# Kernel tuning notes

Hardware: AMD Instinct MI355X
Metric: run time of the kernel (lower is better)

Reference implementation:

```python
import jax, jax.numpy as jnp
import numpy as np

BOARD_H, BOARD_W = 10, 9
NUM_NODES = BOARD_H * BOARD_W  # 90
NUM_HEADS = 4


def _build_base_adjacency():
    adj = np.zeros((NUM_NODES, NUM_NODES), dtype=np.float32)
    for y in range(BOARD_H):
        for x in range(BOARD_W):
            idx = y * BOARD_W + x
            for dy, dx in [(0, 1), (0, -1), (1, 0), (-1, 0)]:
                ny, nx = y + dy, x + dx
                if 0 <= ny < BOARD_H and 0 <= nx < BOARD_W:
                    adj[idx, ny * BOARD_W + nx] = 1.0
            for nx in range(BOARD_W):
                if nx != x and abs(nx - x) <= 4:
                    nidx = y * BOARD_W + nx
                    adj[idx, nidx] = max(adj[idx, nidx], 1.0 / abs(nx - x))
            for ny in range(BOARD_H):
                if ny != y and abs(ny - y) <= 5:
                    nidx = ny * BOARD_W + x
                    adj[idx, nidx] = max(adj[idx, nidx], 1.0 / abs(ny - y))
            adj[idx, idx] = 1.0
    deg = np.clip(adj.sum(-1, keepdims=True), 1.0, None)
    return adj / deg  # (90, 90)


def _pos_encoding():
    px = (np.arange(BOARD_W, dtype=np.float32) / BOARD_W)
    py = (np.arange(BOARD_H, dtype=np.float32) / BOARD_H)
    gx = np.broadcast_to(px[None, :], (BOARD_H, BOARD_W)).reshape(-1)
    gy = np.broadcast_to(py[:, None], (BOARD_H, BOARD_W)).reshape(-1)
    return np.stack([gx, gy], axis=-1)  # (90, 2)


def _gat_layer(x, adj, W, a_src, a_dst, gamma, beta):
    B, N, _ = x.shape
    h = (x @ W).reshape(B, N, NUM_HEADS, -1)          # (B,N,H,D)
    s_src = jnp.einsum('bnhd,hd->bhn', h, a_src)       # (B,H,N)
    s_dst = jnp.einsum('bnhd,hd->bhn', h, a_dst)
    attn = s_src[..., :, None] + s_dst[..., None, :]   # (B,H,N,N)
    attn = jax.nn.leaky_relu(attn, 0.2)
    attn = jnp.where((adj == 0)[None, None], -jnp.inf, attn)
    attn = jax.nn.softmax(attn, axis=-1)
    attn = jnp.nan_to_num(attn, nan=0.0)
    out = jnp.einsum('bhij,bjhd->bihd', attn, h).reshape(B * N, -1)
    # BatchNorm1d in training mode: biased batch stats over (B*N)
    mean = out.mean(0)
    var = out.var(0)
    out = (out - mean) * jax.lax.rsqrt(var + 1e-5) * gamma + beta
    return jax.nn.relu(out.reshape(B, N, -1))


def setup_inputs() -> dict:
    key = jax.random.key(0)
    ks = jax.random.split(key, 16)
    B, F_in, Hd, Dout = 2048, 16, 64, 128
    hdim = Hd // NUM_HEADS
    p = lambda k, s: (jax.random.normal(k, s, dtype=jnp.float32) * 0.1)
    return {
        'board_planes': jax.random.uniform(ks[0], (B, 14, BOARD_H, BOARD_W), dtype=jnp.float32),
        'in_W': p(ks[1], (F_in, Hd)), 'in_b': p(ks[2], (Hd,)),
        'W0': p(ks[3], (Hd, Hd)), 'asrc0': p(ks[4], (NUM_HEADS, hdim)), 'adst0': p(ks[5], (NUM_HEADS, hdim)),
        'g0': jnp.ones((Hd,), jnp.float32), 'b0': jnp.zeros((Hd,), jnp.float32),
        'W1': p(ks[6], (Hd, Hd)), 'asrc1': p(ks[7], (NUM_HEADS, hdim)), 'adst1': p(ks[8], (NUM_HEADS, hdim)),
        'g1': jnp.ones((Hd,), jnp.float32), 'b1': jnp.zeros((Hd,), jnp.float32),
        'out_W': p(ks[9], (Hd, Dout)), 'out_b': p(ks[10], (Dout,)),
    }


def reference(board_planes, in_W, in_b, W0, asrc0, adst0, g0, b0,
              W1, asrc1, adst1, g1, b1, out_W, out_b):
    B = board_planes.shape[0]
    adj = jnp.asarray(_build_base_adjacency())            # (90,90), same for all batches
    nodes = board_planes.reshape(B, 14, NUM_NODES).transpose(0, 2, 1)  # (B,90,14)
    pos = jnp.broadcast_to(jnp.asarray(_pos_encoding())[None], (B, NUM_NODES, 2))
    x = jnp.concatenate([nodes, pos], axis=-1)            # (B,90,16)
    x = x @ in_W + in_b
    x = _gat_layer(x, adj, W0, asrc0, adst0, g0, b0)
    x = _gat_layer(x, adj, W1, asrc1, adst1, g1, b1)
    return x.mean(axis=1) @ out_W + out_b                 # (B,128)
```

## Files before the change

kernel.cpp:

```cpp
#include <hip/hip_runtime.h>
#include <cstdint>


#define BB   2048
#define NN   90
#define NP   96
#define CC   64
#define NH   4
#define HD   16
#define TPB  512
#define DOUT 128
#define SXP  72
#define SWP  72
#define PPITCH 20
#define NSLOT 19

typedef _Float16 f16;
typedef _Float16 f16x4 __attribute__((ext_vector_type(4)));
typedef _Float16 f16x8 __attribute__((ext_vector_type(8)));
typedef float f32x4 __attribute__((ext_vector_type(4)));
union U16x4 { f16x4 v; f16 e[4]; };
union U16x8 { f16x8 v; f16 e[8]; };


template <int LAYER>
__global__ __launch_bounds__(TPB, 6) void k_gat(
    const float* __restrict__ bp,
    const float* __restrict__ inW,
    const float* __restrict__ inb,
    const f16*   __restrict__ prevPre,
    const float* __restrict__ stPrev,
    const float* __restrict__ Wl,
    const float* __restrict__ asrc,
    const float* __restrict__ adst,
    f16*   __restrict__ outPre,
    float* __restrict__ partial,
    float* __restrict__ partialSq)
{
    __shared__ __align__(16) unsigned char big[13824];
    __shared__ __align__(16) unsigned char uni[19712];
    __shared__ float sAs[NH * HD], sAd[NH * HD];
    __shared__ float sSrc[NH][NN], sDst[NH][NN];
    __shared__ float sST[2 * CC];

    f16*   sx   = (f16*)big;
    f16*   sh16 = (f16*)big;
    f16*   sWt  = (f16*)uni;
    float* sInW = (float*)(uni + 9216);
    float* sInb = (float*)(uni + 13312);
    float* sXr  = (float*)(uni + 13568);
    f16*   sPh  = (f16*)uni;
    float* sRa  = (float*)uni;
    float* sRb  = (float*)(uni + 8192);

    const int b = blockIdx.x, t = threadIdx.x;
    const int cq = t & 15, ng = t >> 4;
    const int c4 = cq << 2;
    const int jcnt = (ng < NN - 64) ? 3 : 2;
    const int lane = t & 63, wv = t >> 6;
    const int lr = lane & 15, lg = lane >> 4;

    for (int i = t; i < CC * CC; i += TPB) {
        int k = i >> 6, c = i & 63;
        sWt[c * SWP + k] = (f16)Wl[i];
    }
    if (t < NH * HD) { sAs[t] = asrc[t]; sAd[t] = adst[t]; }
    if (t < (NP - NN) * (SXP / 4)) {
        int r = t / (SXP / 4), q = t - r * (SXP / 4);
        f16x4 z = {(f16)0, (f16)0, (f16)0, (f16)0};
        *(f16x4*)&sx[(NN + r) * SXP + q * 4] = z;
    }
    if (LAYER == 0) {
        for (int i = t; i < 16 * CC; i += TPB) sInW[i] = inW[i];
        if (t < CC) sInb[t] = inb[t];
        const float* bpb = bp + (size_t)b * (14 * NN);
        for (int i = t; i < 14 * NN; i += TPB) {
            int p = i / NN, n = i - p * NN;
            sXr[n * 17 + p] = bpb[i];
        }
        if (t < NN) {
            int y = t / 9, x = t - y * 9;
            sXr[t * 17 + 14] = (float)x / 9.0f;
            sXr[t * 17 + 15] = (float)y / 10.0f;
        }
    } else {
        if (t < 2 * CC) sST[t] = stPrev[t];
    }
    __syncthreads();

    if (LAYER == 0) {
        const int n0 = ng, n1 = ng + 32, n2 = (jcnt == 3) ? ng + 64 : ng;
        float acc[3][4] = {};
        #pragma unroll 4
        for (int k = 0; k < 16; k++) {
            float4 w = *(const float4*)&sInW[k * CC + c4];
            float x0 = sXr[n0 * 17 + k], x1 = sXr[n1 * 17 + k], x2 = sXr[n2 * 17 + k];
            acc[0][0] = fmaf(x0, w.x, acc[0][0]); acc[0][1] = fmaf(x0, w.y, acc[0][1]);
            acc[0][2] = fmaf(x0, w.z, acc[0][2]); acc[0][3] = fmaf(x0, w.w, acc[0][3]);
            acc[1][0] = fmaf(x1, w.x, acc[1][0]); acc[1][1] = fmaf(x1, w.y, acc[1][1]);
            acc[1][2] = fmaf(x1, w.z, acc[1][2]); acc[1][3] = fmaf(x1, w.w, acc[1][3]);
            acc[2][0] = fmaf(x2, w.x, acc[2][0]); acc[2][1] = fmaf(x2, w.y, acc[2][1]);
            acc[2][2] = fmaf(x2, w.z, acc[2][2]); acc[2][3] = fmaf(x2, w.w, acc[2][3]);
        }
        float4 bias = *(const float4*)&sInb[c4];
        for (int j = 0; j < jcnt; j++) {
            int n = ng + 32 * j;
            f16x4 o;
            o.x = (f16)(acc[j][0] + bias.x);
            o.y = (f16)(acc[j][1] + bias.y);
            o.z = (f16)(acc[j][2] + bias.z);
            o.w = (f16)(acc[j][3] + bias.w);
            *(f16x4*)&sx[n * SXP + c4] = o;
        }
    } else {
        const f16x8* pv8 = (const f16x8*)(prevPre + (size_t)b * (NN * CC));
        for (int i8 = t; i8 < NN * CC / 8; i8 += TPB) {
            U16x8 v; v.v = pv8[i8];
            int n = i8 >> 3, c8 = (i8 & 7) << 3;
            U16x8 o;
            #pragma unroll
            for (int j = 0; j < 8; j++) {
                float a = fmaf((float)v.e[j], sST[c8 + j], sST[CC + c8 + j]);
                o.e[j] = (f16)(a > 0.0f ? a : 0.0f);
            }
            *(f16x8*)&sx[n * SXP + c8] = o.v;
        }
    }
    __syncthreads();

    {
        const int nt = wv & 3, m0 = wv >> 2;
        const f16x8 bf0 = *(const f16x8*)&sWt[(nt * 16 + lr) * SWP + lg * 8];
        const f16x8 bf1 = *(const f16x8*)&sWt[(nt * 16 + lr) * SWP + 32 + lg * 8];
        f16x8 af0[3], af1[3];
        #pragma unroll
        for (int mi = 0; mi < 3; mi++) {
            const int mt = m0 + 2 * mi;
            af0[mi] = *(const f16x8*)&sx[(mt * 16 + lr) * SXP + lg * 8];
            af1[mi] = *(const f16x8*)&sx[(mt * 16 + lr) * SXP + 32 + lg * 8];
        }
        __syncthreads();
        #pragma unroll
        for (int mi = 0; mi < 3; mi++) {
            const int mt = m0 + 2 * mi;
            f32x4 acc = {0.0f, 0.0f, 0.0f, 0.0f};
            acc = __builtin_amdgcn_mfma_f32_16x16x32_f16(af0[mi], bf0, acc, 0, 0, 0);
            acc = __builtin_amdgcn_mfma_f32_16x16x32_f16(af1[mi], bf1, acc, 0, 0, 0);
            const int row = mt * 16 + lg * 4, col = nt * 16 + lr;
            #pragma unroll
            for (int r = 0; r < 4; r++)
                sh16[(row + r) * SXP + col] = (f16)acc[r];
        }
    }
    __syncthreads();

    if (t < NH * NN) {
        int hh = t / NN, n = t - hh * NN;
        U16x8 h0, h1;
        h0.v = *(const f16x8*)&sh16[n * SXP + hh * HD];
        h1.v = *(const f16x8*)&sh16[n * SXP + hh * HD + 8];
        float a = 0.0f, d = 0.0f;
        #pragma unroll
        for (int j = 0; j < 8; j++) {
            a = fmaf((float)h0.e[j], sAs[hh * HD + j], a);
            a = fmaf((float)h1.e[j], sAs[hh * HD + 8 + j], a);
            d = fmaf((float)h0.e[j], sAd[hh * HD + j], d);
            d = fmaf((float)h1.e[j], sAd[hh * HD + 8 + j], d);
        }
        sSrc[hh][n] = a; sDst[hh][n] = d;
    }
    __syncthreads();

    if (t < NH * NN) {
        int hh = t / NN, n = t - hh * NN;
        int y = n / 9, x = n - y * 9;
        float si = sSrc[hh][n];
        float e[NSLOT];
        #pragma unroll
        for (int xx = 0; xx < 9; xx++) {
            int dx = xx > x ? xx - x : x - xx;
            float ee = si + sDst[hh][y * 9 + xx];
            ee = ee > 0.0f ? ee : 0.2f * ee;
            e[xx] = (dx <= 4) ? ee : -1e30f;
        }
        #pragma unroll
        for (int yy = 0; yy < 10; yy++) {
            int dy = yy > y ? yy - y : y - yy;
            float ee = si + sDst[hh][yy * 9 + x];
            ee = ee > 0.0f ? ee : 0.2f * ee;
            e[9 + yy] = (dy >= 1 && dy <= 5) ? ee : -1e30f;
        }
        float m = e[0];
        #pragma unroll
        for (int k = 1; k < NSLOT; k++) m = fmaxf(m, e[k]);
        float p[NSLOT];
        float s = 0.0f;
        #pragma unroll
        for (int k = 0; k < NSLOT; k++) { p[k] = __expf(e[k] - m); s += p[k]; }
        float inv = 1.0f / s;
        f16* pr = &sPh[t * PPITCH];
        #pragma unroll
        for (int q = 0; q < 5; q++) {
            U16x4 o;
            #pragma unroll
            for (int j = 0; j < 4; j++) {
                int k = 4 * q + j;
                o.e[j] = (k < NSLOT) ? (f16)(p[k] * inv) : (f16)0;
            }
            *(f16x4*)&pr[4 * q] = o.v;
        }
    }
    __syncthreads();

    const int hh2 = cq >> 2;
    float lsum[4] = {}, lsq[4] = {};
    f16* op = outPre + (size_t)b * (NN * CC);
    for (int j = 0; j < jcnt; j++) {
        int n = ng + 32 * j;
        int y = n / 9, x = n - y * 9;
        const f16* pr = &sPh[(hh2 * NN + n) * PPITCH];
        U16x4 P0, P1, P2, P3, P4;
        P0.v = *(const f16x4*)&pr[0];
        P1.v = *(const f16x4*)&pr[4];
        P2.v = *(const f16x4*)&pr[8];
        P3.v = *(const f16x4*)&pr[12];
        P4.v = *(const f16x4*)&pr[16];
        float a0 = 0.0f, a1 = 0.0f, a2 = 0.0f, a3 = 0.0f;
        #pragma unroll
        for (int xx = 0; xx < 9; xx++) {
            float p = (xx < 4) ? (float)P0.e[xx]
                    : (xx < 8) ? (float)P1.e[xx - 4] : (float)P2.e[0];
            U16x4 h4; h4.v = *(const f16x4*)&sh16[(y * 9 + xx) * SXP + c4];
            a0 = fmaf((float)h4.e[0], p, a0); a1 = fmaf((float)h4.e[1], p, a1);
            a2 = fmaf((float)h4.e[2], p, a2); a3 = fmaf((float)h4.e[3], p, a3);
        }
        #pragma unroll
        for (int yy = 0; yy < 10; yy++) {
            int k = 9 + yy;
            float p = (k < 12) ? (float)P2.e[k - 8]
                    : (k < 16) ? (float)P3.e[k - 12] : (float)P4.e[k - 16];
            U16x4 h4; h4.v = *(const f16x4*)&sh16[(yy * 9 + x) * SXP + c4];
            a0 = fmaf((float)h4.e[0], p, a0); a1 = fmaf((float)h4.e[1], p, a1);
            a2 = fmaf((float)h4.e[2], p, a2); a3 = fmaf((float)h4.e[3], p, a3);
        }
        U16x4 o;
        o.e[0] = (f16)a0; o.e[1] = (f16)a1; o.e[2] = (f16)a2; o.e[3] = (f16)a3;
        *(f16x4*)&op[n * CC + c4] = o.v;
        float r0 = (float)o.e[0], r1 = (float)o.e[1];
        float r2 = (float)o.e[2], r3 = (float)o.e[3];
        lsum[0] += r0; lsum[1] += r1; lsum[2] += r2; lsum[3] += r3;
        lsq[0] = fmaf(r0, r0, lsq[0]); lsq[1] = fmaf(r1, r1, lsq[1]);
        lsq[2] = fmaf(r2, r2, lsq[2]); lsq[3] = fmaf(r3, r3, lsq[3]);
    }
    __syncthreads();

    #pragma unroll
    for (int q = 0; q < 4; q++) {
        sRa[ng * CC + c4 + q] = lsum[q];
        sRb[ng * CC + c4 + q] = lsq[q];
    }
    __syncthreads();
    if (t < CC) {
        float s = 0.0f, q2 = 0.0f;
        #pragma unroll
        for (int g = 0; g < 32; g++) {
            s  += sRa[g * CC + t];
            q2 += sRb[g * CC + t];
        }
        partial[(size_t)b * CC + t] = s;
        partialSq[(size_t)b * CC + t] = q2;
    }
}

__global__ __launch_bounds__(256) void k_stats(
    const float* __restrict__ partial, const float* __restrict__ partialSq,
    const float* __restrict__ gamma, const float* __restrict__ beta,
    float* __restrict__ st)
{
    const int c = blockIdx.x, t = threadIdx.x;
    float s = 0.0f, q = 0.0f;
    for (int b = t; b < BB; b += 256) {
        s += partial[(size_t)b * CC + c];
        q += partialSq[(size_t)b * CC + c];
    }
    __shared__ float rs[256], rq[256];
    rs[t] = s; rq[t] = q;
    __syncthreads();
    for (int o = 128; o > 0; o >>= 1) {
        if (t < o) { rs[t] += rs[t + o]; rq[t] += rq[t + o]; }
        __syncthreads();
    }
    if (t == 0) {
        const float cntInv = 1.0f / (float)(BB * NN);
        float mean = rs[0] * cntInv;
        float var  = rq[0] * cntInv - mean * mean;
        float sc = gamma[c] * rsqrtf(var + 1e-5f);
        st[c] = sc;
        st[CC + c] = beta[c] - mean * sc;
    }
}

__global__ __launch_bounds__(256) void k_final(
    const f16* __restrict__ pre, const float* __restrict__ st,
    const float* __restrict__ outW, const float* __restrict__ outb,
    float* __restrict__ out)
{
    __shared__ float sM[CC];
    __shared__ float sPart[4][CC];
    const int b = blockIdx.x, t = threadIdx.x;
    const int c = t & 63, p = t >> 6;
    const f16* pv = pre + (size_t)b * (NN * CC);
    float s = st[c], sft = st[CC + c];
    float a = 0.0f;
    int nBeg = p * 23, nEnd = nBeg + 23 < NN ? nBeg + 23 : NN;
    for (int n = nBeg; n < nEnd; n++) {
        float v = fmaf((float)pv[n * CC + c], s, sft);
        a += (v > 0.0f ? v : 0.0f);
    }
    sPart[p][c] = a;
    __syncthreads();
    if (t < CC)
        sM[t] = (sPart[0][t] + sPart[1][t] + sPart[2][t] + sPart[3][t]) * (1.0f / (float)NN);
    __syncthreads();
    if (t < DOUT) {
        float acc = outb[t];
        #pragma unroll
        for (int cc2 = 0; cc2 < CC; cc2++) acc = fmaf(sM[cc2], outW[cc2 * DOUT + t], acc);
        out[(size_t)b * DOUT + t] = acc;
    }
}

extern "C" void kernel_launch(void* const* d_in, const int* in_sizes, int n_in,
                              void* d_out, int out_size, void* d_ws, size_t ws_size,
                              hipStream_t stream) {
    (void)in_sizes; (void)n_in; (void)out_size; (void)ws_size;

    const float* bp   = (const float*)d_in[0];
    const float* inW  = (const float*)d_in[1];
    const float* inb  = (const float*)d_in[2];
    const float* W0   = (const float*)d_in[3];
    const float* as0  = (const float*)d_in[4];
    const float* ad0  = (const float*)d_in[5];
    const float* g0   = (const float*)d_in[6];
    const float* b0   = (const float*)d_in[7];
    const float* W1   = (const float*)d_in[8];
    const float* as1  = (const float*)d_in[9];
    const float* ad1  = (const float*)d_in[10];
    const float* g1   = (const float*)d_in[11];
    const float* b1   = (const float*)d_in[12];
    const float* outW = (const float*)d_in[13];
    const float* outb = (const float*)d_in[14];
    float* out = (float*)d_out;

    unsigned char* ws = (unsigned char*)d_ws;
    f16*   outPre    = (f16*)ws;
    float* partial   = (float*)(ws + 23592960);
    float* partialSq = (float*)(ws + 23592960 + 524288);
    float* st0       = (float*)(ws + 23592960 + 1048576);
    float* st1       = st0 + 2 * CC;

    k_gat<0><<<BB, TPB, 0, stream>>>(bp, inW, inb, nullptr, nullptr,
                                     W0, as0, ad0, outPre, partial, partialSq);
    k_stats<<<CC, 256, 0, stream>>>(partial, partialSq, g0, b0, st0);
    k_gat<1><<<BB, TPB, 0, stream>>>(nullptr, nullptr, nullptr, outPre, st0,
                                     W1, as1, ad1, outPre, partial, partialSq);
    k_stats<<<CC, 256, 0, stream>>>(partial, partialSq, g1, b1, st1);
    k_final<<<BB, 256, 0, stream>>>(outPre, st1, outW, outb, out);
}
```

Baseline: 111.0 us.

## Process two boards per GAT block and reduce BN partials with wave shuffles

Each GAT block now handles two batch elements, so the weight transpose/convert and parameter loads are amortized over twice the work and the grid is halved. LDS is merged into one buffer sized for two boards, and launch bounds drop from 6 to 4 waves-per-SIMD hint, lowering occupancy. The per-channel sum/sumsq reduction now uses cross-lane shuffles before a smaller LDS reduction. The g1 rename is cosmetic.

```diff
diff --git a/kernel.cpp b/kernel.cpp
--- a/kernel.cpp
+++ b/kernel.cpp
@@ -9,6 +9,7 @@
 #define NH   4
 #define HD   16
 #define TPB  512
+#define GRID (BB / 2)
 #define DOUT 128
 #define SXP  72
 #define SWP  72
@@ -22,9 +23,10 @@
 union U16x4 { f16x4 v; f16 e[4]; };
 union U16x8 { f16x8 v; f16 e[8]; };
 
+#define LDS_BYTES 63232
 
 template <int LAYER>
-__global__ __launch_bounds__(TPB, 6) void k_gat(
+__global__ __launch_bounds__(TPB, 4) void k_gat(
     const float* __restrict__ bp,
     const float* __restrict__ inW,
     const float* __restrict__ inb,
@@ -37,23 +39,24 @@
     float* __restrict__ partial,
     float* __restrict__ partialSq)
 {
-    __shared__ __align__(16) unsigned char big[13824];
-    __shared__ __align__(16) unsigned char uni[19712];
-    __shared__ float sAs[NH * HD], sAd[NH * HD];
-    __shared__ float sSrc[NH][NN], sDst[NH][NN];
-    __shared__ float sST[2 * CC];
-
-    f16*   sx   = (f16*)big;
-    f16*   sh16 = (f16*)big;
-    f16*   sWt  = (f16*)uni;
-    float* sInW = (float*)(uni + 9216);
-    float* sInb = (float*)(uni + 13312);
-    float* sXr  = (float*)(uni + 13568);
-    f16*   sPh  = (f16*)uni;
-    float* sRa  = (float*)uni;
-    float* sRb  = (float*)(uni + 8192);
-
-    const int b = blockIdx.x, t = threadIdx.x;
+    __shared__ __align__(16) unsigned char lds[LDS_BYTES];
+    f16*   sxA  = (f16*)lds;
+    f16*   sxB  = (f16*)(lds + 13824);
+    f16*   sWt  = (f16*)(lds + 27648);
+    float* sInW = (float*)(lds + 36864);
+    float* sInb = (float*)(lds + 40960);
+    float* sXrA = (float*)(lds + 41216);
+    float* sXrB = (float*)(lds + 47336);
+    f16*   sPh  = (f16*)(lds + 27648);
+    float* sRa  = (float*)(lds + 27648);
+    float* sRb  = (float*)(lds + 31744);
+    float* sSrc = (float*)(lds + 56448);
+    float* sDst = (float*)(lds + 59328);
+    float* sAs  = (float*)(lds + 62208);
+    float* sAd  = (float*)(lds + 62464);
+    float* sST  = (float*)(lds + 62720);
+
+    const int b2 = blockIdx.x * 2, t = threadIdx.x;
     const int cq = t & 15, ng = t >> 4;
     const int c4 = cq << 2;
     const int jcnt = (ng < NN - 64) ? 3 : 2;
@@ -65,23 +68,29 @@
         sWt[c * SWP + k] = (f16)Wl[i];
     }
     if (t < NH * HD) { sAs[t] = asrc[t]; sAd[t] = adst[t]; }
-    if (t < (NP - NN) * (SXP / 4)) {
-        int r = t / (SXP / 4), q = t - r * (SXP / 4);
+    if (t < 2 * (NP - NN) * (SXP / 4)) {
+        int u = t;
+        int g = u / 108; u -= g * 108;
+        int r = u / 18, q = u - r * 18;
         f16x4 z = {(f16)0, (f16)0, (f16)0, (f16)0};
+        f16* sx = g ? sxB : sxA;
         *(f16x4*)&sx[(NN + r) * SXP + q * 4] = z;
     }
     if (LAYER == 0) {
         for (int i = t; i < 16 * CC; i += TPB) sInW[i] = inW[i];
         if (t < CC) sInb[t] = inb[t];
-        const float* bpb = bp + (size_t)b * (14 * NN);
-        for (int i = t; i < 14 * NN; i += TPB) {
-            int p = i / NN, n = i - p * NN;
-            sXr[n * 17 + p] = bpb[i];
-        }
-        if (t < NN) {
-            int y = t / 9, x = t - y * 9;
-            sXr[t * 17 + 14] = (float)x / 9.0f;
-            sXr[t * 17 + 15] = (float)y / 10.0f;
+        for (int i = t; i < 2 * 14 * NN; i += TPB) {
+            int g = i / 1260, r = i - g * 1260;
+            int p = r / NN, n = r - p * NN;
+            float v = bp[(size_t)(b2 + g) * 1260 + r];
+            (g ? sXrB : sXrA)[n * 17 + p] = v;
+        }
+        if (t < 2 * NN) {
+            int g = t / NN, n = t - g * NN;
+            int y = n / 9, x = n - y * 9;
+            float* X = g ? sXrB : sXrA;
+            X[n * 17 + 14] = (float)x / 9.0f;
+            X[n * 17 + 15] = (float)y / 10.0f;
         }
     } else {
         if (t < 2 * CC) sST[t] = stPrev[t];
@@ -89,41 +98,50 @@
     __syncthreads();
 
     if (LAYER == 0) {
-        const int n0 = ng, n1 = ng + 32, n2 = (jcnt == 3) ? ng + 64 : ng;
-        float acc[3][4] = {};
-        #pragma unroll 4
-        for (int k = 0; k < 16; k++) {
-            float4 w = *(const float4*)&sInW[k * CC + c4];
-            float x0 = sXr[n0 * 17 + k], x1 = sXr[n1 * 17 + k], x2 = sXr[n2 * 17 + k];
-            acc[0][0] = fmaf(x0, w.x, acc[0][0]); acc[0][1] = fmaf(x0, w.y, acc[0][1]);
-            acc[0][2] = fmaf(x0, w.z, acc[0][2]); acc[0][3] = fmaf(x0, w.w, acc[0][3]);
-            acc[1][0] = fmaf(x1, w.x, acc[1][0]); acc[1][1] = fmaf(x1, w.y, acc[1][1]);
-            acc[1][2] = fmaf(x1, w.z, acc[1][2]); acc[1][3] = fmaf(x1, w.w, acc[1][3]);
-            acc[2][0] = fmaf(x2, w.x, acc[2][0]); acc[2][1] = fmaf(x2, w.y, acc[2][1]);
-            acc[2][2] = fmaf(x2, w.z, acc[2][2]); acc[2][3] = fmaf(x2, w.w, acc[2][3]);
-        }
-        float4 bias = *(const float4*)&sInb[c4];
-        for (int j = 0; j < jcnt; j++) {
-            int n = ng + 32 * j;
-            f16x4 o;
-            o.x = (f16)(acc[j][0] + bias.x);
-            o.y = (f16)(acc[j][1] + bias.y);
-            o.z = (f16)(acc[j][2] + bias.z);
-            o.w = (f16)(acc[j][3] + bias.w);
-            *(f16x4*)&sx[n * SXP + c4] = o;
+        #pragma unroll
+        for (int g = 0; g < 2; g++) {
+            const float* sXr = g ? sXrB : sXrA;
+            f16* sx = g ? sxB : sxA;
+            const int n0 = ng, n1 = ng + 32, n2 = (jcnt == 3) ? ng + 64 : ng;
+            float acc[3][4] = {};
+            #pragma unroll 4
+            for (int k = 0; k < 16; k++) {
+                float4 w = *(const float4*)&sInW[k * CC + c4];
+                float x0 = sXr[n0 * 17 + k], x1 = sXr[n1 * 17 + k], x2 = sXr[n2 * 17 + k];
+                acc[0][0] = fmaf(x0, w.x, acc[0][0]); acc[0][1] = fmaf(x0, w.y, acc[0][1]);
+                acc[0][2] = fmaf(x0, w.z, acc[0][2]); acc[0][3] = fmaf(x0, w.w, acc[0][3]);
+                acc[1][0] = fmaf(x1, w.x, acc[1][0]); acc[1][1] = fmaf(x1, w.y, acc[1][1]);
+                acc[1][2] = fmaf(x1, w.z, acc[1][2]); acc[1][3] = fmaf(x1, w.w, acc[1][3]);
+                acc[2][0] = fmaf(x2, w.x, acc[2][0]); acc[2][1] = fmaf(x2, w.y, acc[2][1]);
+                acc[2][2] = fmaf(x2, w.z, acc[2][2]); acc[2][3] = fmaf(x2, w.w, acc[2][3]);
+            }
+            float4 bias = *(const float4*)&sInb[c4];
+            for (int j = 0; j < jcnt; j++) {
+                int n = ng + 32 * j;
+                f16x4 o;
+                o.x = (f16)(acc[j][0] + bias.x);
+                o.y = (f16)(acc[j][1] + bias.y);
+                o.z = (f16)(acc[j][2] + bias.z);
+                o.w = (f16)(acc[j][3] + bias.w);
+                *(f16x4*)&sx[n * SXP + c4] = o;
+            }
         }
     } else {
-        const f16x8* pv8 = (const f16x8*)(prevPre + (size_t)b * (NN * CC));
-        for (int i8 = t; i8 < NN * CC / 8; i8 += TPB) {
-            U16x8 v; v.v = pv8[i8];
-            int n = i8 >> 3, c8 = (i8 & 7) << 3;
-            U16x8 o;
-            #pragma unroll
-            for (int j = 0; j < 8; j++) {
-                float a = fmaf((float)v.e[j], sST[c8 + j], sST[CC + c8 + j]);
-                o.e[j] = (f16)(a > 0.0f ? a : 0.0f);
-            }
-            *(f16x8*)&sx[n * SXP + c8] = o.v;
+        #pragma unroll
+        for (int g = 0; g < 2; g++) {
+            const f16x8* pv8 = (const f16x8*)(prevPre + (size_t)(b2 + g) * (NN * CC));
+            f16* sx = g ? sxB : sxA;
+            for (int i8 = t; i8 < NN * CC / 8; i8 += TPB) {
+                U16x8 v; v.v = pv8[i8];
+                int n = i8 >> 3, c8 = (i8 & 7) << 3;
+                U16x8 o;
+                #pragma unroll
+                for (int j = 0; j < 8; j++) {
+                    float a = fmaf((float)v.e[j], sST[c8 + j], sST[CC + c8 + j]);
+                    o.e[j] = (f16)(a > 0.0f ? a : 0.0f);
+                }
+                *(f16x8*)&sx[n * SXP + c8] = o.v;
+            }
         }
     }
     __syncthreads();
@@ -132,33 +150,43 @@
         const int nt = wv & 3, m0 = wv >> 2;
         const f16x8 bf0 = *(const f16x8*)&sWt[(nt * 16 + lr) * SWP + lg * 8];
         const f16x8 bf1 = *(const f16x8*)&sWt[(nt * 16 + lr) * SWP + 32 + lg * 8];
-        f16x8 af0[3], af1[3];
+        f16x8 aA0[3], aA1[3], aB0[3], aB1[3];
         #pragma unroll
         for (int mi = 0; mi < 3; mi++) {
             const int mt = m0 + 2 * mi;
-            af0[mi] = *(const f16x8*)&sx[(mt * 16 + lr) * SXP + lg * 8];
-            af1[mi] = *(const f16x8*)&sx[(mt * 16 + lr) * SXP + 32 + lg * 8];
+            aA0[mi] = *(const f16x8*)&sxA[(mt * 16 + lr) * SXP + lg * 8];
+            aA1[mi] = *(const f16x8*)&sxA[(mt * 16 + lr) * SXP + 32 + lg * 8];
+            aB0[mi] = *(const f16x8*)&sxB[(mt * 16 + lr) * SXP + lg * 8];
+            aB1[mi] = *(const f16x8*)&sxB[(mt * 16 + lr) * SXP + 32 + lg * 8];
         }
         __syncthreads();
         #pragma unroll
         for (int mi = 0; mi < 3; mi++) {
             const int mt = m0 + 2 * mi;
-            f32x4 acc = {0.0f, 0.0f, 0.0f, 0.0f};
-            acc = __builtin_amdgcn_mfma_f32_16x16x32_f16(af0[mi], bf0, acc, 0, 0, 0);
-            acc = __builtin_amdgcn_mfma_f32_16x16x32_f16(af1[mi], bf1, acc, 0, 0, 0);
             const int row = mt * 16 + lg * 4, col = nt * 16 + lr;
+            f32x4 accA = {0.0f, 0.0f, 0.0f, 0.0f};
+            accA = __builtin_amdgcn_mfma_f32_16x16x32_f16(aA0[mi], bf0, accA, 0, 0, 0);
+            accA = __builtin_amdgcn_mfma_f32_16x16x32_f16(aA1[mi], bf1, accA, 0, 0, 0);
             #pragma unroll
             for (int r = 0; r < 4; r++)
-                sh16[(row + r) * SXP + col] = (f16)acc[r];
-        }
-    }
-    __syncthreads();
-
-    if (t < NH * NN) {
-        int hh = t / NN, n = t - hh * NN;
+                sxA[(row + r) * SXP + col] = (f16)accA[r];
+            f32x4 accB = {0.0f, 0.0f, 0.0f, 0.0f};
+            accB = __builtin_amdgcn_mfma_f32_16x16x32_f16(aB0[mi], bf0, accB, 0, 0, 0);
+            accB = __builtin_amdgcn_mfma_f32_16x16x32_f16(aB1[mi], bf1, accB, 0, 0, 0);
+            #pragma unroll
+            for (int r = 0; r < 4; r++)
+                sxB[(row + r) * SXP + col] = (f16)accB[r];
+        }
+    }
+    __syncthreads();
+
+    for (int i = t; i < 2 * NH * NN; i += TPB) {
+        int g = i / (NH * NN), r = i - g * (NH * NN);
+        int hh = r / NN, n = r - hh * NN;
+        const f16* sh = g ? sxB : sxA;
         U16x8 h0, h1;
-        h0.v = *(const f16x8*)&sh16[n * SXP + hh * HD];
-        h1.v = *(const f16x8*)&sh16[n * SXP + hh * HD + 8];
+        h0.v = *(const f16x8*)&sh[n * SXP + hh * HD];
+        h1.v = *(const f16x8*)&sh[n * SXP + hh * HD + 8];
         float a = 0.0f, d = 0.0f;
         #pragma unroll
         for (int j = 0; j < 8; j++) {
@@ -167,26 +195,28 @@
             d = fmaf((float)h0.e[j], sAd[hh * HD + j], d);
             d = fmaf((float)h1.e[j], sAd[hh * HD + 8 + j], d);
         }
-        sSrc[hh][n] = a; sDst[hh][n] = d;
-    }
-    __syncthreads();
-
-    if (t < NH * NN) {
-        int hh = t / NN, n = t - hh * NN;
+        sSrc[i] = a; sDst[i] = d;
+    }
+    __syncthreads();
+
+    for (int i = t; i < 2 * NH * NN; i += TPB) {
+        int g = i / (NH * NN), r = i - g * (NH * NN);
+        int hh = r / NN, n = r - hh * NN;
         int y = n / 9, x = n - y * 9;
-        float si = sSrc[hh][n];
+        float si = sSrc[i];
+        const float* dst = &sDst[(g * NH + hh) * NN];
         float e[NSLOT];
         #pragma unroll
         for (int xx = 0; xx < 9; xx++) {
             int dx = xx > x ? xx - x : x - xx;
-            float ee = si + sDst[hh][y * 9 + xx];
+            float ee = si + dst[y * 9 + xx];
             ee = ee > 0.0f ? ee : 0.2f * ee;
             e[xx] = (dx <= 4) ? ee : -1e30f;
         }
         #pragma unroll
         for (int yy = 0; yy < 10; yy++) {
             int dy = yy > y ? yy - y : y - yy;
-            float ee = si + sDst[hh][yy * 9 + x];
+            float ee = si + dst[yy * 9 + x];
             ee = ee > 0.0f ? ee : 0.2f * ee;
             e[9 + yy] = (dy >= 1 && dy <= 5) ? ee : -1e30f;
         }
@@ -198,7 +228,7 @@
         #pragma unroll
         for (int k = 0; k < NSLOT; k++) { p[k] = __expf(e[k] - m); s += p[k]; }
         float inv = 1.0f / s;
-        f16* pr = &sPh[t * PPITCH];
+        f16* pr = &sPh[i * PPITCH];
         #pragma unroll
         for (int q = 0; q < 5; q++) {
             U16x4 o;
@@ -213,62 +243,84 @@
     __syncthreads();
 
     const int hh2 = cq >> 2;
-    float lsum[4] = {}, lsq[4] = {};
-    f16* op = outPre + (size_t)b * (NN * CC);
-    for (int j = 0; j < jcnt; j++) {
-        int n = ng + 32 * j;
-        int y = n / 9, x = n - y * 9;
-        const f16* pr = &sPh[(hh2 * NN + n) * PPITCH];
-        U16x4 P0, P1, P2, P3, P4;
-        P0.v = *(const f16x4*)&pr[0];
-        P1.v = *(const f16x4*)&pr[4];
-        P2.v = *(const f16x4*)&pr[8];
-        P3.v = *(const f16x4*)&pr[12];
-        P4.v = *(const f16x4*)&pr[16];
-        float a0 = 0.0f, a1 = 0.0f, a2 = 0.0f, a3 = 0.0f;
-        #pragma unroll
-        for (int xx = 0; xx < 9; xx++) {
-            float p = (xx < 4) ? (float)P0.e[xx]
-                    : (xx < 8) ? (float)P1.e[xx - 4] : (float)P2.e[0];
-            U16x4 h4; h4.v = *(const f16x4*)&sh16[(y * 9 + xx) * SXP + c4];
-            a0 = fmaf((float)h4.e[0], p, a0); a1 = fmaf((float)h4.e[1], p, a1);
-            a2 = fmaf((float)h4.e[2], p, a2); a3 = fmaf((float)h4.e[3], p, a3);
-        }
-        #pragma unroll
-        for (int yy = 0; yy < 10; yy++) {
-            int k = 9 + yy;
-            float p = (k < 12) ? (float)P2.e[k - 8]
-                    : (k < 16) ? (float)P3.e[k - 12] : (float)P4.e[k - 16];
-            U16x4 h4; h4.v = *(const f16x4*)&sh16[(yy * 9 + x) * SXP + c4];
-            a0 = fmaf((float)h4.e[0], p, a0); a1 = fmaf((float)h4.e[1], p, a1);
-            a2 = fmaf((float)h4.e[2], p, a2); a3 = fmaf((float)h4.e[3], p, a3);
-        }
-        U16x4 o;
-        o.e[0] = (f16)a0; o.e[1] = (f16)a1; o.e[2] = (f16)a2; o.e[3] = (f16)a3;
-        *(f16x4*)&op[n * CC + c4] = o.v;
-        float r0 = (float)o.e[0], r1 = (float)o.e[1];
-        float r2 = (float)o.e[2], r3 = (float)o.e[3];
-        lsum[0] += r0; lsum[1] += r1; lsum[2] += r2; lsum[3] += r3;
-        lsq[0] = fmaf(r0, r0, lsq[0]); lsq[1] = fmaf(r1, r1, lsq[1]);
-        lsq[2] = fmaf(r2, r2, lsq[2]); lsq[3] = fmaf(r3, r3, lsq[3]);
-    }
-    __syncthreads();
-
+    float lsum[2][4] = {}, lsq[2][4] = {};
     #pragma unroll
-    for (int q = 0; q < 4; q++) {
-        sRa[ng * CC + c4 + q] = lsum[q];
-        sRb[ng * CC + c4 + q] = lsq[q];
-    }
-    __syncthreads();
-    if (t < CC) {
+    for (int g = 0; g < 2; g++) {
+        const f16* sh = g ? sxB : sxA;
+        const f16* phBase = &sPh[g * (NH * NN) * PPITCH];
+        f16* op = outPre + (size_t)(b2 + g) * (NN * CC);
+        for (int j = 0; j < jcnt; j++) {
+            int n = ng + 32 * j;
+            int y = n / 9, x = n - y * 9;
+            const f16* pr = &phBase[(hh2 * NN + n) * PPITCH];
+            U16x4 P0, P1, P2, P3, P4;
+            P0.v = *(const f16x4*)&pr[0];
+            P1.v = *(const f16x4*)&pr[4];
+            P2.v = *(const f16x4*)&pr[8];
+            P3.v = *(const f16x4*)&pr[12];
+            P4.v = *(const f16x4*)&pr[16];
+            float a0 = 0.0f, a1 = 0.0f, a2 = 0.0f, a3 = 0.0f;
+            #pragma unroll
+            for (int xx = 0; xx < 9; xx++) {
+                float p = (xx < 4) ? (float)P0.e[xx]
+                        : (xx < 8) ? (float)P1.e[xx - 4] : (float)P2.e[0];
+                U16x4 h4; h4.v = *(const f16x4*)&sh[(y * 9 + xx) * SXP + c4];
+                a0 = fmaf((float)h4.e[0], p, a0); a1 = fmaf((float)h4.e[1], p, a1);
+                a2 = fmaf((float)h4.e[2], p, a2); a3 = fmaf((float)h4.e[3], p, a3);
+            }
+            #pragma unroll
+            for (int yy = 0; yy < 10; yy++) {
+                int k = 9 + yy;
+                float p = (k < 12) ? (float)P2.e[k - 8]
+                        : (k < 16) ? (float)P3.e[k - 12] : (float)P4.e[k - 16];
+                U16x4 h4; h4.v = *(const f16x4*)&sh[(yy * 9 + x) * SXP + c4];
+                a0 = fmaf((float)h4.e[0], p, a0); a1 = fmaf((float)h4.e[1], p, a1);
+                a2 = fmaf((float)h4.e[2], p, a2); a3 = fmaf((float)h4.e[3], p, a3);
+            }
+            U16x4 o;
+            o.e[0] = (f16)a0; o.e[1] = (f16)a1; o.e[2] = (f16)a2; o.e[3] = (f16)a3;
+            *(f16x4*)&op[n * CC + c4] = o.v;
+            float r0 = (float)o.e[0], r1 = (float)o.e[1];
+            float r2 = (float)o.e[2], r3 = (float)o.e[3];
+            lsum[g][0] += r0; lsum[g][1] += r1; lsum[g][2] += r2; lsum[g][3] += r3;
+            lsq[g][0] = fmaf(r0, r0, lsq[g][0]); lsq[g][1] = fmaf(r1, r1, lsq[g][1]);
+            lsq[g][2] = fmaf(r2, r2, lsq[g][2]); lsq[g][3] = fmaf(r3, r3, lsq[g][3]);
+        }
+    }
+    __syncthreads();
+
+    #pragma unroll
+    for (int g = 0; g < 2; g++) {
+        #pragma unroll
+        for (int q = 0; q < 4; q++) {
+            float v = lsum[g][q];
+            v += __shfl_xor(v, 16); v += __shfl_xor(v, 32);
+            lsum[g][q] = v;
+            float w2 = lsq[g][q];
+            w2 += __shfl_xor(w2, 16); w2 += __shfl_xor(w2, 32);
+            lsq[g][q] = w2;
+        }
+    }
+    if (lg == 0) {
+        #pragma unroll
+        for (int g = 0; g < 2; g++) {
+            float4 a; a.x = lsum[g][0]; a.y = lsum[g][1]; a.z = lsum[g][2]; a.w = lsum[g][3];
+            float4 c; c.x = lsq[g][0];  c.y = lsq[g][1];  c.z = lsq[g][2];  c.w = lsq[g][3];
+            *(float4*)&sRa[(g * 8 + wv) * CC + lr * 4] = a;
+            *(float4*)&sRb[(g * 8 + wv) * CC + lr * 4] = c;
+        }
+    }
+    __syncthreads();
+    if (t < 2 * CC) {
+        int g = t >> 6, c = t & 63;
         float s = 0.0f, q2 = 0.0f;
         #pragma unroll
-        for (int g = 0; g < 32; g++) {
-            s  += sRa[g * CC + t];
-            q2 += sRb[g * CC + t];
-        }
-        partial[(size_t)b * CC + t] = s;
-        partialSq[(size_t)b * CC + t] = q2;
+        for (int w = 0; w < 8; w++) {
+            s  += sRa[(g * 8 + w) * CC + c];
+            q2 += sRb[(g * 8 + w) * CC + c];
+        }
+        partial[(size_t)(b2 + g) * CC + c] = s;
+        partialSq[(size_t)(b2 + g) * CC + c] = q2;
     }
 }
 
@@ -346,7 +398,7 @@
     const float* W1   = (const float*)d_in[8];
     const float* as1  = (const float*)d_in[9];
     const float* ad1  = (const float*)d_in[10];
-    const float* g1   = (const float*)d_in[11];
+    const float* b1g  = (const float*)d_in[11];
     const float* b1   = (const float*)d_in[12];
     const float* outW = (const float*)d_in[13];
     const float* outb = (const float*)d_in[14];
@@ -359,11 +411,11 @@
     float* st0       = (float*)(ws + 23592960 + 1048576);
     float* st1       = st0 + 2 * CC;
 
-    k_gat<0><<<BB, TPB, 0, stream>>>(bp, inW, inb, nullptr, nullptr,
-                                     W0, as0, ad0, outPre, partial, partialSq);
+    k_gat<0><<<GRID, TPB, 0, stream>>>(bp, inW, inb, nullptr, nullptr,
+                                       W0, as0, ad0, outPre, partial, partialSq);
     k_stats<<<CC, 256, 0, stream>>>(partial, partialSq, g0, b0, st0);
-    k_gat<1><<<BB, TPB, 0, stream>>>(nullptr, nullptr, nullptr, outPre, st0,
-                                     W1, as1, ad1, outPre, partial, partialSq);
-    k_stats<<<CC, 256, 0, stream>>>(partial, partialSq, g1, b1, st1);
+    k_gat<1><<<GRID, TPB, 0, stream>>>(nullptr, nullptr, nullptr, outPre, st0,
+                                       W1, as1, ad1, outPre, partial, partialSq);
+    k_stats<<<CC, 256, 0, stream>>>(partial, partialSq, b1g, b1, st1);
     k_final<<<BB, 256, 0, stream>>>(outPre, st1, outW, outb, out);
 }
```

Measured after the change: 119.5 us. 1.08x slower.

## Fuse softmax with aggregation per head-node thread and shrink block to six waves

Applied to the files above, without the earlier changes.

Each (node, head) thread now computes the softmax and immediately accumulates the 16-channel weighted sum of neighbour features, so the fp16 probability buffer and its separate aggregation pass with an extra barrier are gone. The block shrinks from 512 to 384 threads, each wave owning one 16-row MFMA tile. In layer 1 the BN-ReLU of the previous layer is applied directly in registers to build the MFMA A fragments. Batch statistics are reduced with warp shuffles instead of a 32-way LDS reduction. The trade-off is more registers per thread, fewer threads active during aggregation (360 of 384), and a lower launch-bounds occupancy target.

```diff
diff --git a/kernel.cpp b/kernel.cpp
--- a/kernel.cpp
+++ b/kernel.cpp
@@ -4,16 +4,13 @@
 
 #define BB   2048
 #define NN   90
-#define NP   96
 #define CC   64
 #define NH   4
 #define HD   16
-#define TPB  512
+#define TPB  384
 #define DOUT 128
 #define SXP  72
 #define SWP  72
-#define PPITCH 20
-#define NSLOT 19
 
 typedef _Float16 f16;
 typedef _Float16 f16x4 __attribute__((ext_vector_type(4)));
@@ -22,9 +19,10 @@
 union U16x4 { f16x4 v; f16 e[4]; };
 union U16x8 { f16x8 v; f16 e[8]; };
 
+#define LDS_BYTES 37440
 
 template <int LAYER>
-__global__ __launch_bounds__(TPB, 6) void k_gat(
+__global__ __launch_bounds__(TPB, 4) void k_gat(
     const float* __restrict__ bp,
     const float* __restrict__ inW,
     const float* __restrict__ inb,
@@ -37,26 +35,20 @@
     float* __restrict__ partial,
     float* __restrict__ partialSq)
 {
-    __shared__ __align__(16) unsigned char big[13824];
-    __shared__ __align__(16) unsigned char uni[19712];
-    __shared__ float sAs[NH * HD], sAd[NH * HD];
-    __shared__ float sSrc[NH][NN], sDst[NH][NN];
-    __shared__ float sST[2 * CC];
-
-    f16*   sx   = (f16*)big;
-    f16*   sh16 = (f16*)big;
-    f16*   sWt  = (f16*)uni;
-    float* sInW = (float*)(uni + 9216);
-    float* sInb = (float*)(uni + 13312);
-    float* sXr  = (float*)(uni + 13568);
-    f16*   sPh  = (f16*)uni;
-    float* sRa  = (float*)uni;
-    float* sRb  = (float*)(uni + 8192);
+    __shared__ __align__(16) unsigned char lds[LDS_BYTES];
+    f16*   sh   = (f16*)lds;
+    f16*   sWt  = (f16*)(lds + 13824);
+    float* sXr  = (float*)(lds + 23040);
+    float* sRed = (float*)(lds + 23040);
+    float* sInW = (float*)(lds + 29184);
+    float* sInb = (float*)(lds + 33280);
+    float* sSrc = (float*)(lds + 33536);
+    float* sDst = (float*)(lds + 34976);
+    float* sAs  = (float*)(lds + 36416);
+    float* sAd  = (float*)(lds + 36672);
+    float* sST  = (float*)(lds + 36928);
 
     const int b = blockIdx.x, t = threadIdx.x;
-    const int cq = t & 15, ng = t >> 4;
-    const int c4 = cq << 2;
-    const int jcnt = (ng < NN - 64) ? 3 : 2;
     const int lane = t & 63, wv = t >> 6;
     const int lr = lane & 15, lg = lane >> 4;
 
@@ -65,14 +57,12 @@
         sWt[c * SWP + k] = (f16)Wl[i];
     }
     if (t < NH * HD) { sAs[t] = asrc[t]; sAd[t] = adst[t]; }
-    if (t < (NP - NN) * (SXP / 4)) {
-        int r = t / (SXP / 4), q = t - r * (SXP / 4);
-        f16x4 z = {(f16)0, (f16)0, (f16)0, (f16)0};
-        *(f16x4*)&sx[(NN + r) * SXP + q * 4] = z;
-    }
     if (LAYER == 0) {
-        for (int i = t; i < 16 * CC; i += TPB) sInW[i] = inW[i];
-        if (t < CC) sInb[t] = inb[t];
+        if (t < 108) {
+            int r = t / 18, q = t - r * 18;
+            f16x4 z = {(f16)0, (f16)0, (f16)0, (f16)0};
+            *(f16x4*)&sh[(NN + r) * SXP + q * 4] = z;
+        }
         const float* bpb = bp + (size_t)b * (14 * NN);
         for (int i = t; i < 14 * NN; i += TPB) {
             int p = i / NN, n = i - p * NN;
@@ -83,82 +73,97 @@
             sXr[t * 17 + 14] = (float)x / 9.0f;
             sXr[t * 17 + 15] = (float)y / 10.0f;
         }
+        for (int i = t; i < 16 * CC; i += TPB) sInW[i] = inW[i];
+        if (t < CC) sInb[t] = inb[t];
     } else {
         if (t < 2 * CC) sST[t] = stPrev[t];
     }
     __syncthreads();
 
     if (LAYER == 0) {
-        const int n0 = ng, n1 = ng + 32, n2 = (jcnt == 3) ? ng + 64 : ng;
-        float acc[3][4] = {};
-        #pragma unroll 4
-        for (int k = 0; k < 16; k++) {
-            float4 w = *(const float4*)&sInW[k * CC + c4];
-            float x0 = sXr[n0 * 17 + k], x1 = sXr[n1 * 17 + k], x2 = sXr[n2 * 17 + k];
-            acc[0][0] = fmaf(x0, w.x, acc[0][0]); acc[0][1] = fmaf(x0, w.y, acc[0][1]);
-            acc[0][2] = fmaf(x0, w.z, acc[0][2]); acc[0][3] = fmaf(x0, w.w, acc[0][3]);
-            acc[1][0] = fmaf(x1, w.x, acc[1][0]); acc[1][1] = fmaf(x1, w.y, acc[1][1]);
-            acc[1][2] = fmaf(x1, w.z, acc[1][2]); acc[1][3] = fmaf(x1, w.w, acc[1][3]);
-            acc[2][0] = fmaf(x2, w.x, acc[2][0]); acc[2][1] = fmaf(x2, w.y, acc[2][1]);
-            acc[2][2] = fmaf(x2, w.z, acc[2][2]); acc[2][3] = fmaf(x2, w.w, acc[2][3]);
-        }
-        float4 bias = *(const float4*)&sInb[c4];
-        for (int j = 0; j < jcnt; j++) {
-            int n = ng + 32 * j;
+        for (int i = t; i < NN * 16; i += TPB) {
+            int n = i >> 4, c4 = (i & 15) << 2;
+            float a0 = 0, a1 = 0, a2 = 0, a3 = 0;
+            #pragma unroll
+            for (int k = 0; k < 16; k++) {
+                float4 w = *(const float4*)&sInW[k * CC + c4];
+                float xv = sXr[n * 17 + k];
+                a0 = fmaf(xv, w.x, a0); a1 = fmaf(xv, w.y, a1);
+                a2 = fmaf(xv, w.z, a2); a3 = fmaf(xv, w.w, a3);
+            }
+            float4 bias = *(const float4*)&sInb[c4];
             f16x4 o;
-            o.x = (f16)(acc[j][0] + bias.x);
-            o.y = (f16)(acc[j][1] + bias.y);
-            o.z = (f16)(acc[j][2] + bias.z);
-            o.w = (f16)(acc[j][3] + bias.w);
-            *(f16x4*)&sx[n * SXP + c4] = o;
-        }
+            o.x = (f16)(a0 + bias.x); o.y = (f16)(a1 + bias.y);
+            o.z = (f16)(a2 + bias.z); o.w = (f16)(a3 + bias.w);
+            *(f16x4*)&sh[n * SXP + c4] = o;
+        }
+        __syncthreads();
+
+        {
+            const int mt = wv;
+            const f16x8 af0 = *(const f16x8*)&sh[(mt * 16 + lr) * SXP + lg * 8];
+            const f16x8 af1 = *(const f16x8*)&sh[(mt * 16 + lr) * SXP + 32 + lg * 8];
+            f16x8 bf0[4], bf1[4];
+            #pragma unroll
+            for (int nt = 0; nt < 4; nt++) {
+                bf0[nt] = *(const f16x8*)&sWt[(nt * 16 + lr) * SWP + lg * 8];
+                bf1[nt] = *(const f16x8*)&sWt[(nt * 16 + lr) * SWP + 32 + lg * 8];
+            }
+            __syncthreads();
+            #pragma unroll
+            for (int nt = 0; nt < 4; nt++) {
+                f32x4 acc = {0.0f, 0.0f, 0.0f, 0.0f};
+                acc = __builtin_amdgcn_mfma_f32_16x16x32_f16(af0, bf0[nt], acc, 0, 0, 0);
+                acc = __builtin_amdgcn_mfma_f32_16x16x32_f16(af1, bf1[nt], acc, 0, 0, 0);
+                const int row = mt * 16 + lg * 4, col = nt * 16 + lr;
+                sh[(row + 0) * SXP + col] = (f16)acc[0];
+                sh[(row + 1) * SXP + col] = (f16)acc[1];
+                sh[(row + 2) * SXP + col] = (f16)acc[2];
+                sh[(row + 3) * SXP + col] = (f16)acc[3];
+            }
+        }
+        __syncthreads();
     } else {
-        const f16x8* pv8 = (const f16x8*)(prevPre + (size_t)b * (NN * CC));
-        for (int i8 = t; i8 < NN * CC / 8; i8 += TPB) {
-            U16x8 v; v.v = pv8[i8];
-            int n = i8 >> 3, c8 = (i8 & 7) << 3;
-            U16x8 o;
+        {
+            const int mt = wv;
+            const int row = mt * 16 + lr;
+            U16x8 va, vb;
+            va.v = (f16x8){};  vb.v = (f16x8){};
+            if (row < NN) {
+                const f16* pp = prevPre + ((size_t)b * NN + row) * CC;
+                va.v = *(const f16x8*)&pp[lg * 8];
+                vb.v = *(const f16x8*)&pp[32 + lg * 8];
+            }
+            U16x8 a0u, a1u;
             #pragma unroll
             for (int j = 0; j < 8; j++) {
-                float a = fmaf((float)v.e[j], sST[c8 + j], sST[CC + c8 + j]);
-                o.e[j] = (f16)(a > 0.0f ? a : 0.0f);
-            }
-            *(f16x8*)&sx[n * SXP + c8] = o.v;
-        }
-    }
-    __syncthreads();
-
-    {
-        const int nt = wv & 3, m0 = wv >> 2;
-        const f16x8 bf0 = *(const f16x8*)&sWt[(nt * 16 + lr) * SWP + lg * 8];
-        const f16x8 bf1 = *(const f16x8*)&sWt[(nt * 16 + lr) * SWP + 32 + lg * 8];
-        f16x8 af0[3], af1[3];
-        #pragma unroll
-        for (int mi = 0; mi < 3; mi++) {
-            const int mt = m0 + 2 * mi;
-            af0[mi] = *(const f16x8*)&sx[(mt * 16 + lr) * SXP + lg * 8];
-            af1[mi] = *(const f16x8*)&sx[(mt * 16 + lr) * SXP + 32 + lg * 8];
+                float v0 = fmaf((float)va.e[j], sST[lg * 8 + j],      sST[64 + lg * 8 + j]);
+                float v1 = fmaf((float)vb.e[j], sST[32 + lg * 8 + j], sST[96 + lg * 8 + j]);
+                a0u.e[j] = (f16)(v0 > 0.0f ? v0 : 0.0f);
+                a1u.e[j] = (f16)(v1 > 0.0f ? v1 : 0.0f);
+            }
+            #pragma unroll
+            for (int nt = 0; nt < 4; nt++) {
+                f16x8 bf0 = *(const f16x8*)&sWt[(nt * 16 + lr) * SWP + lg * 8];
+                f16x8 bf1 = *(const f16x8*)&sWt[(nt * 16 + lr) * SWP + 32 + lg * 8];
+                f32x4 acc = {0.0f, 0.0f, 0.0f, 0.0f};
+                acc = __builtin_amdgcn_mfma_f32_16x16x32_f16(a0u.v, bf0, acc, 0, 0, 0);
+                acc = __builtin_amdgcn_mfma_f32_16x16x32_f16(a1u.v, bf1, acc, 0, 0, 0);
+                const int orow = mt * 16 + lg * 4, col = nt * 16 + lr;
+                sh[(orow + 0) * SXP + col] = (f16)acc[0];
+                sh[(orow + 1) * SXP + col] = (f16)acc[1];
+                sh[(orow + 2) * SXP + col] = (f16)acc[2];
+                sh[(orow + 3) * SXP + col] = (f16)acc[3];
+            }
         }
         __syncthreads();
-        #pragma unroll
-        for (int mi = 0; mi < 3; mi++) {
-            const int mt = m0 + 2 * mi;
-            f32x4 acc = {0.0f, 0.0f, 0.0f, 0.0f};
-            acc = __builtin_amdgcn_mfma_f32_16x16x32_f16(af0[mi], bf0, acc, 0, 0, 0);
-            acc = __builtin_amdgcn_mfma_f32_16x16x32_f16(af1[mi], bf1, acc, 0, 0, 0);
-            const int row = mt * 16 + lg * 4, col = nt * 16 + lr;
-            #pragma unroll
-            for (int r = 0; r < 4; r++)
-                sh16[(row + r) * SXP + col] = (f16)acc[r];
-        }
-    }
-    __syncthreads();
+    }
 
     if (t < NH * NN) {
-        int hh = t / NN, n = t - hh * NN;
+        int hh = t & 3, n = t >> 2;
         U16x8 h0, h1;
-        h0.v = *(const f16x8*)&sh16[n * SXP + hh * HD];
-        h1.v = *(const f16x8*)&sh16[n * SXP + hh * HD + 8];
+        h0.v = *(const f16x8*)&sh[n * SXP + hh * HD];
+        h1.v = *(const f16x8*)&sh[n * SXP + hh * HD + 8];
         float a = 0.0f, d = 0.0f;
         #pragma unroll
         for (int j = 0; j < 8; j++) {
@@ -167,108 +172,108 @@
             d = fmaf((float)h0.e[j], sAd[hh * HD + j], d);
             d = fmaf((float)h1.e[j], sAd[hh * HD + 8 + j], d);
         }
-        sSrc[hh][n] = a; sDst[hh][n] = d;
-    }
-    __syncthreads();
-
+        sSrc[hh * NN + n] = a;
+        sDst[hh * NN + n] = d;
+    }
+    __syncthreads();
+
+    float sum[16], sq[16];
+    #pragma unroll
+    for (int q = 0; q < 16; q++) { sum[q] = 0.0f; sq[q] = 0.0f; }
     if (t < NH * NN) {
-        int hh = t / NN, n = t - hh * NN;
-        int y = n / 9, x = n - y * 9;
-        float si = sSrc[hh][n];
-        float e[NSLOT];
+        const int hh = t & 3, n = t >> 2;
+        const int y = n / 9, x = n - y * 9;
+        const float si = sSrc[hh * NN + n];
+        const float* dst = &sDst[hh * NN];
+        float e[19];
         #pragma unroll
         for (int xx = 0; xx < 9; xx++) {
             int dx = xx > x ? xx - x : x - xx;
-            float ee = si + sDst[hh][y * 9 + xx];
+            float ee = si + dst[y * 9 + xx];
             ee = ee > 0.0f ? ee : 0.2f * ee;
             e[xx] = (dx <= 4) ? ee : -1e30f;
         }
         #pragma unroll
         for (int yy = 0; yy < 10; yy++) {
             int dy = yy > y ? yy - y : y - yy;
-            float ee = si + sDst[hh][yy * 9 + x];
+            float ee = si + dst[yy * 9 + x];
             ee = ee > 0.0f ? ee : 0.2f * ee;
             e[9 + yy] = (dy >= 1 && dy <= 5) ? ee : -1e30f;
         }
         float m = e[0];
         #pragma unroll
-        for (int k = 1; k < NSLOT; k++) m = fmaxf(m, e[k]);
-        float p[NSLOT];
+        for (int k = 1; k < 19; k++) m = fmaxf(m, e[k]);
+        float acc[16];
+        #pragma unroll
+        for (int q = 0; q < 16; q++) acc[q] = 0.0f;
         float s = 0.0f;
         #pragma unroll
-        for (int k = 0; k < NSLOT; k++) { p[k] = __expf(e[k] - m); s += p[k]; }
+        for (int k = 0; k < 19; k++) {
+            float p = __expf(e[k] - m);
+            s += p;
+            int j = (k < 9) ? (y * 9 + k) : ((k - 9) * 9 + x);
+            U16x8 h0, h1;
+            h0.v = *(const f16x8*)&sh[j * SXP + hh * HD];
+            h1.v = *(const f16x8*)&sh[j * SXP + hh * HD + 8];
+            #pragma unroll
+            for (int q = 0; q < 8; q++) {
+                acc[q]     = fmaf((float)h0.e[q], p, acc[q]);
+                acc[8 + q] = fmaf((float)h1.e[q], p, acc[8 + q]);
+            }
+        }
         float inv = 1.0f / s;
-        f16* pr = &sPh[t * PPITCH];
-        #pragma unroll
-        for (int q = 0; q < 5; q++) {
-            U16x4 o;
-            #pragma unroll
-            for (int j = 0; j < 4; j++) {
-                int k = 4 * q + j;
-                o.e[j] = (k < NSLOT) ? (f16)(p[k] * inv) : (f16)0;
-            }
-            *(f16x4*)&pr[4 * q] = o.v;
-        }
-    }
-    __syncthreads();
-
-    const int hh2 = cq >> 2;
-    float lsum[4] = {}, lsq[4] = {};
-    f16* op = outPre + (size_t)b * (NN * CC);
-    for (int j = 0; j < jcnt; j++) {
-        int n = ng + 32 * j;
-        int y = n / 9, x = n - y * 9;
-        const f16* pr = &sPh[(hh2 * NN + n) * PPITCH];
-        U16x4 P0, P1, P2, P3, P4;
-        P0.v = *(const f16x4*)&pr[0];
-        P1.v = *(const f16x4*)&pr[4];
-        P2.v = *(const f16x4*)&pr[8];
-        P3.v = *(const f16x4*)&pr[12];
-        P4.v = *(const f16x4*)&pr[16];
-        float a0 = 0.0f, a1 = 0.0f, a2 = 0.0f, a3 = 0.0f;
-        #pragma unroll
-        for (int xx = 0; xx < 9; xx++) {
-            float p = (xx < 4) ? (float)P0.e[xx]
-                    : (xx < 8) ? (float)P1.e[xx - 4] : (float)P2.e[0];
-            U16x4 h4; h4.v = *(const f16x4*)&sh16[(y * 9 + xx) * SXP + c4];
-            a0 = fmaf((float)h4.e[0], p, a0); a1 = fmaf((float)h4.e[1], p, a1);
-            a2 = fmaf((float)h4.e[2], p, a2); a3 = fmaf((float)h4.e[3], p, a3);
-        }
-        #pragma unroll
-        for (int yy = 0; yy < 10; yy++) {
-            int k = 9 + yy;
-            float p = (k < 12) ? (float)P2.e[k - 8]
-                    : (k < 16) ? (float)P3.e[k - 12] : (float)P4.e[k - 16];
-            U16x4 h4; h4.v = *(const f16x4*)&sh16[(yy * 9 + x) * SXP + c4];
-            a0 = fmaf((float)h4.e[0], p, a0); a1 = fmaf((float)h4.e[1], p, a1);
-            a2 = fmaf((float)h4.e[2], p, a2); a3 = fmaf((float)h4.e[3], p, a3);
-        }
-        U16x4 o;
-        o.e[0] = (f16)a0; o.e[1] = (f16)a1; o.e[2] = (f16)a2; o.e[3] = (f16)a3;
-        *(f16x4*)&op[n * CC + c4] = o.v;
-        float r0 = (float)o.e[0], r1 = (float)o.e[1];
-        float r2 = (float)o.e[2], r3 = (float)o.e[3];
-        lsum[0] += r0; lsum[1] += r1; lsum[2] += r2; lsum[3] += r3;
-        lsq[0] = fmaf(r0, r0, lsq[0]); lsq[1] = fmaf(r1, r1, lsq[1]);
-        lsq[2] = fmaf(r2, r2, lsq[2]); lsq[3] = fmaf(r3, r3, lsq[3]);
-    }
-    __syncthreads();
-
+        U16x8 o0, o1;
+        #pragma unroll
+        for (int q = 0; q < 8; q++) {
+            o0.e[q] = (f16)(acc[q] * inv);
+            o1.e[q] = (f16)(acc[8 + q] * inv);
+        }
+        f16* op = outPre + ((size_t)b * NN + n) * CC + hh * HD;
+        *(f16x8*)op = o0.v;
+        *(f16x8*)(op + 8) = o1.v;
+        #pragma unroll
+        for (int q = 0; q < 8; q++) {
+            float r0 = (float)o0.e[q], r1 = (float)o1.e[q];
+            sum[q] = r0;     sq[q] = r0 * r0;
+            sum[8 + q] = r1; sq[8 + q] = r1 * r1;
+        }
+    }
     #pragma unroll
-    for (int q = 0; q < 4; q++) {
-        sRa[ng * CC + c4 + q] = lsum[q];
-        sRb[ng * CC + c4 + q] = lsq[q];
-    }
-    __syncthreads();
+    for (int q = 0; q < 16; q++) {
+        float v = sum[q];
+        v += __shfl_xor(v, 4); v += __shfl_xor(v, 8);
+        v += __shfl_xor(v, 16); v += __shfl_xor(v, 32);
+        sum[q] = v;
+        float w2 = sq[q];
+        w2 += __shfl_xor(w2, 4); w2 += __shfl_xor(w2, 8);
+        w2 += __shfl_xor(w2, 16); w2 += __shfl_xor(w2, 32);
+        sq[q] = w2;
+    }
+    if (lane < 4) {
+        float* dstp = &sRed[(wv * 4 + lane) * 32];
+        #pragma unroll
+        for (int q4 = 0; q4 < 4; q4++) {
+            float4 a, c;
+            a.x = sum[q4 * 4 + 0]; a.y = sum[q4 * 4 + 1];
+            a.z = sum[q4 * 4 + 2]; a.w = sum[q4 * 4 + 3];
+            c.x = sq[q4 * 4 + 0];  c.y = sq[q4 * 4 + 1];
+            c.z = sq[q4 * 4 + 2];  c.w = sq[q4 * 4 + 3];
+            *(float4*)&dstp[q4 * 4] = a;
+            *(float4*)&dstp[16 + q4 * 4] = c;
+        }
+    }
+    __syncthreads();
+
     if (t < CC) {
-        float s = 0.0f, q2 = 0.0f;
-        #pragma unroll
-        for (int g = 0; g < 32; g++) {
-            s  += sRa[g * CC + t];
-            q2 += sRb[g * CC + t];
+        int hh = t >> 4, q = t & 15;
+        float s = 0.0f, ss = 0.0f;
+        #pragma unroll
+        for (int w = 0; w < 6; w++) {
+            s  += sRed[(w * 4 + hh) * 32 + q];
+            ss += sRed[(w * 4 + hh) * 32 + 16 + q];
         }
         partial[(size_t)b * CC + t] = s;
-        partialSq[(size_t)b * CC + t] = q2;
+        partialSq[(size_t)b * CC + t] = ss;
     }
 }
 
```

Result: slower. 173.3 us (+56.2%).
